# Optimization experiments

Measured on AMD Instinct MI355X. Metric: run time of the kernel, lower is better.

Reference implementation:

```python
import jax, jax.numpy as jnp
import numpy as np

B, T, L = 256, 1024, 128  # batch, seq_len, num_labels


def setup_inputs() -> dict:
    key = jax.random.key(0)
    k1, k2, k3, k4, k5 = jax.random.split(key, 5)
    h = jax.random.normal(k1, (B, T, L), dtype=jnp.float32)
    labels = jax.random.randint(k2, (B, T), 0, L)
    mask = jnp.ones((B, T), dtype=jnp.float32)
    u = lambda k, s: jax.random.uniform(k, s, jnp.float32, -0.1, 0.1)
    trans_matrix = u(k3, (L, L))
    start_trans = u(k4, (L,))
    end_trans = u(k5, (L,))
    return {"h": h, "labels": labels, "mask": mask,
            "trans_matrix": trans_matrix, "start_trans": start_trans,
            "end_trans": end_trans}


def reference(h, labels, mask, trans_matrix, start_trans, end_trans):
    # ---- numerator: score of the gold path ----
    h_y = jnp.take_along_axis(h, labels[..., None], axis=2)[..., 0]      # (B,T)
    trans_y = trans_matrix[labels[:, :-1], labels[:, 1:]]                # (B,T-1)
    num = start_trans[labels[:, 0]]
    num = num + jnp.sum(h_y[:, :-1] * mask[:, :-1] + trans_y * mask[:, 1:], axis=1)
    last_idx = mask.astype(jnp.int32).sum(axis=1) - 1                    # (B,)
    last_labels = jnp.take_along_axis(labels, last_idx[:, None], axis=1)[:, 0]
    # original torch code gathers from h[:, -1] (last timestep), keep faithful
    num = num + jnp.take_along_axis(h[:, -1], last_labels[:, None], axis=1)[:, 0] * mask[:, -1]
    num = num + end_trans[last_labels]

    # ---- denominator: log partition via scan over time ----
    def step(score, inp):
        h_t, m_t = inp  # (B,L), (B,)
        s = jax.nn.logsumexp(score[:, :, None] + h_t[:, None, :] + trans_matrix[None], axis=1)
        m = m_t[:, None]
        return s * m + score * (1.0 - m), None

    score0 = start_trans[None, :] + h[:, 0]                              # (B,L)
    hs = jnp.swapaxes(h, 0, 1)[1:]                                       # (T-1,B,L)
    ms = mask.T[1:]                                                      # (T-1,B)
    scoreT, _ = jax.lax.scan(step, score0, (hs, ms))
    den = jax.nn.logsumexp(scoreT + end_trans[None, :], axis=1)          # (B,)

    return num - den
```

## Files before the change

### kernel.cpp

```cpp
#include <hip/hip_runtime.h>
#include <math.h>

#define Bb 256
#define Tt 1024
#define Ll 128

typedef float v2f __attribute__((ext_vector_type(2)));

__global__ __launch_bounds__(256) void crf_expT_kernel(
    const float* __restrict__ trans, float* __restrict__ expT)
{
    int idx = blockIdx.x * 256 + threadIdx.x;
    if (idx < Ll * Ll) {
        int jj = idx >> 7;
        int ii = idx & (Ll - 1);
        expT[idx] = __expf(trans[ii * Ll + jj]);
    }
}

__global__ __launch_bounds__(256) void crf_num_kernel(
    const float* __restrict__ h, const int* __restrict__ labels,
    const float* __restrict__ mask, const float* __restrict__ trans,
    const float* __restrict__ start_trans, const float* __restrict__ end_trans,
    float* __restrict__ num_out)
{
    const int b = blockIdx.x;
    const int tid = threadIdx.x;
    const int* lab = labels + b * Tt;
    const float* mk = mask + b * Tt;
    const float* hb = h + (size_t)b * Tt * Ll;

    float acc = 0.f;
    float msum = 0.f;
    for (int t = tid; t < Tt; t += 256) {
        int lt = lab[t];
        float mt = mk[t];
        msum += mt;
        if (t < Tt - 1) {
            int lt1 = lab[t + 1];
            acc += hb[t * Ll + lt] * mt + trans[lt * Ll + lt1] * mk[t + 1];
        }
    }
    for (int off = 32; off; off >>= 1) {
        acc  += __shfl_down(acc, off, 64);
        msum += __shfl_down(msum, off, 64);
    }
    __shared__ float racc[4], rmsum[4];
    const int wave = tid >> 6;
    if ((tid & 63) == 0) { racc[wave] = acc; rmsum[wave] = msum; }
    __syncthreads();
    if (tid == 0) {
        float a = racc[0] + racc[1] + racc[2] + racc[3];
        float m = rmsum[0] + rmsum[1] + rmsum[2] + rmsum[3];
        int last_idx = (int)(m + 0.5f) - 1;
        if (last_idx < 0) last_idx = 0;
        if (last_idx > Tt - 1) last_idx = Tt - 1;
        int last_lab = lab[last_idx];
        float num = a + start_trans[lab[0]];
        num += hb[(Tt - 1) * Ll + last_lab] * mk[Tt - 1];
        num += end_trans[last_lab];
        num_out[b] = num;
    }
}

__global__ __launch_bounds__(256)
__attribute__((amdgpu_waves_per_eu(1, 1)))
void crf_den_kernel(
    const float* __restrict__ h, const float* __restrict__ mask,
    const float* __restrict__ expT, const float* __restrict__ start_trans,
    const float* __restrict__ end_trans, const float* __restrict__ num_in,
    float* __restrict__ out)
{
    __shared__ float p_lds[2][160];
    __shared__ float mk_lds[Tt];
    __shared__ float redm[4], reds[4];

    const int b = blockIdx.x;
    const int tid = threadIdx.x;
    const int wave = tid >> 6;
    const int lane = tid & 63;
    const int jgrp = lane >> 3;
    const int isl  = lane & 7;
    const int jbase = (wave << 5) + (jgrp << 2);
    const int wcol  = jbase + (isl & 3);
    const bool writer = (isl < 4);
    const int waddr = wcol + ((wcol >> 4) << 2);
    const bool lb0 = (lane & 1) != 0;
    const bool lb1 = (lane & 2) != 0;

    const float* hb = h + (size_t)b * Tt * Ll;
    const float* mk = mask + b * Tt;

    ((float4*)mk_lds)[tid] = ((const float4*)mk)[tid];

    const v2f* EAp = (const v2f*)(expT + (jbase + 0) * Ll + (isl << 4));
    const v2f* EBp = (const v2f*)(expT + (jbase + 1) * Ll + (isl << 4));
    const v2f* ECp = (const v2f*)(expT + (jbase + 2) * Ll + (isl << 4));
    const v2f* EDp = (const v2f*)(expT + (jbase + 3) * Ll + (isl << 4));
    v2f EA0=EAp[0],EA1=EAp[1],EA2=EAp[2],EA3=EAp[3],EA4=EAp[4],EA5=EAp[5],EA6=EAp[6],EA7=EAp[7];
    v2f EB0=EBp[0],EB1=EBp[1],EB2=EBp[2],EB3=EBp[3],EB4=EBp[4],EB5=EBp[5],EB6=EBp[6],EB7=EBp[7];
    v2f EC0=ECp[0],EC1=ECp[1],EC2=ECp[2],EC3=ECp[3],EC4=ECp[4],EC5=ECp[5],EC6=ECp[6],EC7=ECp[7];
    v2f ED0=EDp[0],ED1=EDp[1],ED2=EDp[2],ED3=EDp[3],ED4=EDp[4],ED5=EDp[5],ED6=EDp[6],ED7=EDp[7];

    float S = start_trans[0] + hb[0] + 16.0f;
    float score0 = start_trans[wcol] + hb[wcol];
    float pw = __expf(score0 - S);
    if (writer) p_lds[0][waddr] = pw;

    float h1 = hb[1 * Ll + wcol], m1 = mk[1];
    float h2 = hb[2 * Ll + wcol], m2 = mk[2];
    float h3 = hb[3 * Ll + wcol], m3 = mk[3];
    float h0 = hb[4 * Ll + wcol], m0 = mk[4];
    __syncthreads();

    float ex1 = __expf(h1) * m1, om1 = 1.f - m1;
    float ex0, om0, ex2, om2, ex3, om3;

#define DPPA(x, ctrl) __int_as_float(__builtin_amdgcn_update_dpp( \
        0, __float_as_int(x), ctrl, 0xF, 0xF, true))

#define BODY(RBUF, UPD, EXc, OMc, HN, MN, EXn, OMn, HR, MR, TR) {      \
    const float4* pp = (const float4*)(&p_lds[RBUF][isl * 20]);        \
    float4 Q0 = pp[0], Q1 = pp[1], Q2 = pp[2], Q3 = pp[3];             \
    float pz = 0.f;                                                    \
    if (UPD) pz = p_lds[RBUF][0];                                      \
    HR = hb[(TR) * Ll + wcol];                                         \
    MR = mk_lds[(TR)];                                                 \
    v2f q00 = {Q0.x,Q0.y}, q01 = {Q0.z,Q0.w};                          \
    v2f q10 = {Q1.x,Q1.y}, q11 = {Q1.z,Q1.w};                          \
    v2f q20 = {Q2.x,Q2.y}, q21 = {Q2.z,Q2.w};                          \
    v2f q30 = {Q3.x,Q3.y}, q31 = {Q3.z,Q3.w};                          \
    v2f A0 = q00*EA0; A0 = q01*EA1 + A0; A0 = q10*EA2 + A0;            \
    A0 = q11*EA3 + A0; A0 = q20*EA4 + A0; A0 = q21*EA5 + A0;           \
    A0 = q30*EA6 + A0; A0 = q31*EA7 + A0;                              \
    v2f A1 = q00*EB0; A1 = q01*EB1 + A1; A1 = q10*EB2 + A1;            \
    A1 = q11*EB3 + A1; A1 = q20*EB4 + A1; A1 = q21*EB5 + A1;           \
    A1 = q30*EB6 + A1; A1 = q31*EB7 + A1;                              \
    v2f A2 = q00*EC0; A2 = q01*EC1 + A2; A2 = q10*EC2 + A2;            \
    A2 = q11*EC3 + A2; A2 = q20*EC4 + A2; A2 = q21*EC5 + A2;           \
    A2 = q30*EC6 + A2; A2 = q31*EC7 + A2;                              \
    v2f A3 = q00*ED0; A3 = q01*ED1 + A3; A3 = q10*ED2 + A3;            \
    A3 = q11*ED3 + A3; A3 = q20*ED4 + A3; A3 = q21*ED5 + A3;           \
    A3 = q30*ED6 + A3; A3 = q31*ED7 + A3;                              \
    float a0 = A0.x + A0.y, a1 = A1.x + A1.y;                          \
    float a2 = A2.x + A2.y, a3 = A3.x + A3.y;                          \
    a0 += DPPA(a0, 0x141); a1 += DPPA(a1, 0x141);                      \
    a2 += DPPA(a2, 0x141); a3 += DPPA(a3, 0x141);                      \
    float u01 = lb0 ? a1 : a0, v01 = lb0 ? a0 : a1;                    \
    float b01 = u01 + DPPA(v01, 0xB1);                                 \
    float u23 = lb0 ? a3 : a2, v23 = lb0 ? a2 : a3;                    \
    float b23 = u23 + DPPA(v23, 0xB1);                                 \
    float uf = lb1 ? b23 : b01, vf = lb1 ? b01 : b23;                  \
    float acc = uf + DPPA(vf, 0x4E);                                   \
    float c1 = EXc, c0 = pw * OMc;                                     \
    if (UPD) { float ed = __fdividef(1.12535175e-7f, pz);              \
               c1 *= ed; c0 *= ed; S += __logf(pz) + 16.0f; }          \
    float pn = fmaf(acc, c1, c0);                                      \
    if (writer) p_lds[(RBUF) ^ 1][waddr] = pn;                         \
    EXn = __expf(HN) * MN; OMn = 1.f - MN;                             \
    pw = pn;                                                           \
    __builtin_amdgcn_sched_barrier(0);                                 \
    asm volatile("s_waitcnt lgkmcnt(0)");                              \
    __builtin_amdgcn_s_barrier();                                      \
    __builtin_amdgcn_sched_barrier(0);                                 \
}

    BODY(0, 0, ex1, om1, h2, m2, ex2, om2, h1, m1, 5)
    BODY(1, 0, ex2, om2, h3, m3, ex3, om3, h2, m2, 6)
    BODY(0, 0, ex3, om3, h0, m0, ex0, om0, h3, m3, 7)

    for (int k = 1; k < 255; ++k) {
        int t4 = k << 2;
        BODY(1, 1, ex0, om0, h1, m1, ex1, om1, h0, m0, t4 + 4)
        BODY(0, 0, ex1, om1, h2, m2, ex2, om2, h1, m1, t4 + 5)
        BODY(1, 0, ex2, om2, h3, m3, ex3, om3, h2, m2, t4 + 6)
        BODY(0, 0, ex3, om3, h0, m0, ex0, om0, h3, m3, t4 + 7)
    }
    BODY(1, 1, ex0, om0, h1, m1, ex1, om1, h0, m0, Tt - 1)
    BODY(0, 0, ex1, om1, h2, m2, ex2, om2, h1, m1, Tt - 1)
    BODY(1, 0, ex2, om2, h3, m3, ex3, om3, h2, m2, Tt - 1)
    BODY(0, 0, ex3, om3, h0, m0, ex0, om0, h3, m3, Tt - 1)
#undef BODY
#undef DPPA

    float v = __logf(pw) + S + end_trans[wcol];
    float mval = writer ? v : -1e30f;
    #pragma unroll
    for (int off = 32; off; off >>= 1) mval = fmaxf(mval, __shfl_xor(mval, off, 64));
    if (lane == 0) redm[wave] = mval;
    __syncthreads();
    float M = fmaxf(fmaxf(redm[0], redm[1]), fmaxf(redm[2], redm[3]));
    float e = writer ? __expf(v - M) : 0.f;
    #pragma unroll
    for (int off = 32; off; off >>= 1) e += __shfl_xor(e, off, 64);
    if (lane == 0) reds[wave] = e;
    __syncthreads();
    if (tid == 0) {
        float den = M + __logf(reds[0] + reds[1] + reds[2] + reds[3]);
        out[b] = num_in[b] - den;
    }
}

extern "C" void kernel_launch(void* const* d_in, const int* in_sizes, int n_in,
                              void* d_out, int out_size, void* d_ws, size_t ws_size,
                              hipStream_t stream) {
    const float* h           = (const float*)d_in[0];
    const int*   labels      = (const int*)d_in[1];
    const float* mask        = (const float*)d_in[2];
    const float* trans       = (const float*)d_in[3];
    const float* start_trans = (const float*)d_in[4];
    const float* end_trans   = (const float*)d_in[5];
    float* out    = (float*)d_out;
    float* num_ws = (float*)d_ws;
    float* expT   = (float*)d_ws + 256;

    crf_expT_kernel<<<(Ll * Ll + 255) / 256, 256, 0, stream>>>(trans, expT);
    crf_num_kernel<<<Bb, 256, 0, stream>>>(h, labels, mask, trans, start_trans, end_trans, num_ws);
    crf_den_kernel<<<Bb, 256, 0, stream>>>(h, mask, expT, start_trans, end_trans, num_ws, out);
}
```

Measured before the change: 264.4 us.

## Fuse exp-transition, numerator and forward-scan kernels into one launch

Merges the three kernels into one. Each block now computes exp(trans) straight from the transition matrix into its register tiles, computes the gold-path numerator before the scan, and reduces it with the denominator at the end. This removes two kernel launches and the workspace round trip for expT and num, at the cost of redundant exp work per block and strided global reads of trans. The scan also loads mask values four at a time as a float4 from LDS instead of one scalar LDS read per step.

After: 247.8 us. 1.07x faster.

```diff
diff --git a/kernel.cpp b/kernel.cpp
--- a/kernel.cpp
+++ b/kernel.cpp
@@ -7,73 +7,19 @@
 
 typedef float v2f __attribute__((ext_vector_type(2)));
 
-__global__ __launch_bounds__(256) void crf_expT_kernel(
-    const float* __restrict__ trans, float* __restrict__ expT)
-{
-    int idx = blockIdx.x * 256 + threadIdx.x;
-    if (idx < Ll * Ll) {
-        int jj = idx >> 7;
-        int ii = idx & (Ll - 1);
-        expT[idx] = __expf(trans[ii * Ll + jj]);
-    }
-}
+__device__ __forceinline__ v2f ev2(float a, float b) { v2f r; r.x = a; r.y = b; return r; }
 
-__global__ __launch_bounds__(256) void crf_num_kernel(
+__global__ __launch_bounds__(256)
+__attribute__((amdgpu_waves_per_eu(1, 1)))
+void crf_fused_kernel(
     const float* __restrict__ h, const int* __restrict__ labels,
     const float* __restrict__ mask, const float* __restrict__ trans,
     const float* __restrict__ start_trans, const float* __restrict__ end_trans,
-    float* __restrict__ num_out)
-{
-    const int b = blockIdx.x;
-    const int tid = threadIdx.x;
-    const int* lab = labels + b * Tt;
-    const float* mk = mask + b * Tt;
-    const float* hb = h + (size_t)b * Tt * Ll;
-
-    float acc = 0.f;
-    float msum = 0.f;
-    for (int t = tid; t < Tt; t += 256) {
-        int lt = lab[t];
-        float mt = mk[t];
-        msum += mt;
-        if (t < Tt - 1) {
-            int lt1 = lab[t + 1];
-            acc += hb[t * Ll + lt] * mt + trans[lt * Ll + lt1] * mk[t + 1];
-        }
-    }
-    for (int off = 32; off; off >>= 1) {
-        acc  += __shfl_down(acc, off, 64);
-        msum += __shfl_down(msum, off, 64);
-    }
-    __shared__ float racc[4], rmsum[4];
-    const int wave = tid >> 6;
-    if ((tid & 63) == 0) { racc[wave] = acc; rmsum[wave] = msum; }
-    __syncthreads();
-    if (tid == 0) {
-        float a = racc[0] + racc[1] + racc[2] + racc[3];
-        float m = rmsum[0] + rmsum[1] + rmsum[2] + rmsum[3];
-        int last_idx = (int)(m + 0.5f) - 1;
-        if (last_idx < 0) last_idx = 0;
-        if (last_idx > Tt - 1) last_idx = Tt - 1;
-        int last_lab = lab[last_idx];
-        float num = a + start_trans[lab[0]];
-        num += hb[(Tt - 1) * Ll + last_lab] * mk[Tt - 1];
-        num += end_trans[last_lab];
-        num_out[b] = num;
-    }
-}
-
-__global__ __launch_bounds__(256)
-__attribute__((amdgpu_waves_per_eu(1, 1)))
-void crf_den_kernel(
-    const float* __restrict__ h, const float* __restrict__ mask,
-    const float* __restrict__ expT, const float* __restrict__ start_trans,
-    const float* __restrict__ end_trans, const float* __restrict__ num_in,
     float* __restrict__ out)
 {
     __shared__ float p_lds[2][160];
-    __shared__ float mk_lds[Tt];
-    __shared__ float redm[4], reds[4];
+    __shared__ float mk_lds[Tt + 4];
+    __shared__ float redm[4], reds[4], racc[4], rmsum[4];
 
     const int b = blockIdx.x;
     const int tid = threadIdx.x;
@@ -90,17 +36,33 @@
 
     const float* hb = h + (size_t)b * Tt * Ll;
     const float* mk = mask + b * Tt;
+    const int* lab = labels + b * Tt;
 
     ((float4*)mk_lds)[tid] = ((const float4*)mk)[tid];
 
-    const v2f* EAp = (const v2f*)(expT + (jbase + 0) * Ll + (isl << 4));
-    const v2f* EBp = (const v2f*)(expT + (jbase + 1) * Ll + (isl << 4));
-    const v2f* ECp = (const v2f*)(expT + (jbase + 2) * Ll + (isl << 4));
-    const v2f* EDp = (const v2f*)(expT + (jbase + 3) * Ll + (isl << 4));
-    v2f EA0=EAp[0],EA1=EAp[1],EA2=EAp[2],EA3=EAp[3],EA4=EAp[4],EA5=EAp[5],EA6=EAp[6],EA7=EAp[7];
-    v2f EB0=EBp[0],EB1=EBp[1],EB2=EBp[2],EB3=EBp[3],EB4=EBp[4],EB5=EBp[5],EB6=EBp[6],EB7=EBp[7];
-    v2f EC0=ECp[0],EC1=ECp[1],EC2=ECp[2],EC3=ECp[3],EC4=ECp[4],EC5=ECp[5],EC6=ECp[6],EC7=ECp[7];
-    v2f ED0=EDp[0],ED1=EDp[1],ED2=EDp[2],ED3=EDp[3],ED4=EDp[4],ED5=EDp[5],ED6=EDp[6],ED7=EDp[7];
+    float nacc = 0.f, nms = 0.f;
+    #pragma unroll
+    for (int r = 0; r < 4; ++r) {
+        int t = tid + (r << 8);
+        float mt = mk[t];
+        nms += mt;
+        if (t < Tt - 1) {
+            int lt = lab[t], lt1 = lab[t + 1];
+            nacc += hb[t * Ll + lt] * mt + trans[lt * Ll + lt1] * mk[t + 1];
+        }
+    }
+
+    const float* tp = trans + (size_t)(isl << 4) * Ll + jbase;
+#define EXT2(k, c) ev2(__expf(tp[(2 * (k)) * Ll + (c)]), __expf(tp[(2 * (k) + 1) * Ll + (c)]))
+    v2f EA0=EXT2(0,0),EA1=EXT2(1,0),EA2=EXT2(2,0),EA3=EXT2(3,0),
+        EA4=EXT2(4,0),EA5=EXT2(5,0),EA6=EXT2(6,0),EA7=EXT2(7,0);
+    v2f EB0=EXT2(0,1),EB1=EXT2(1,1),EB2=EXT2(2,1),EB3=EXT2(3,1),
+        EB4=EXT2(4,1),EB5=EXT2(5,1),EB6=EXT2(6,1),EB7=EXT2(7,1);
+    v2f EC0=EXT2(0,2),EC1=EXT2(1,2),EC2=EXT2(2,2),EC3=EXT2(3,2),
+        EC4=EXT2(4,2),EC5=EXT2(5,2),EC6=EXT2(6,2),EC7=EXT2(7,2);
+    v2f ED0=EXT2(0,3),ED1=EXT2(1,3),ED2=EXT2(2,3),ED3=EXT2(3,3),
+        ED4=EXT2(4,3),ED5=EXT2(5,3),ED6=EXT2(6,3),ED7=EXT2(7,3);
+#undef EXT2
 
     float S = start_trans[0] + hb[0] + 16.0f;
     float score0 = start_trans[wcol] + hb[wcol];
@@ -115,17 +77,19 @@
 
     float ex1 = __expf(h1) * m1, om1 = 1.f - m1;
     float ex0, om0, ex2, om2, ex3, om3;
+    float4 MQ;
 
 #define DPPA(x, ctrl) __int_as_float(__builtin_amdgcn_update_dpp( \
         0, __float_as_int(x), ctrl, 0xF, 0xF, true))
 
-#define BODY(RBUF, UPD, EXc, OMc, HN, MN, EXn, OMn, HR, MR, TR) {      \
+#define BODY(RBUF, UPD, EXc, OMc, HN, MN, EXn, OMn, HR, MR, TR, MV, LQ) {  \
     const float4* pp = (const float4*)(&p_lds[RBUF][isl * 20]);        \
     float4 Q0 = pp[0], Q1 = pp[1], Q2 = pp[2], Q3 = pp[3];             \
     float pz = 0.f;                                                    \
     if (UPD) pz = p_lds[RBUF][0];                                      \
     HR = hb[(TR) * Ll + wcol];                                         \
-    MR = mk_lds[(TR)];                                                 \
+    MR = (MV);                                                         \
+    if (LQ) MQ = *(const float4*)(&mk_lds[(TR) + 1]);                  \
     v2f q00 = {Q0.x,Q0.y}, q01 = {Q0.z,Q0.w};                          \
     v2f q10 = {Q1.x,Q1.y}, q11 = {Q1.z,Q1.w};                          \
     v2f q20 = {Q2.x,Q2.y}, q21 = {Q2.z,Q2.w};                          \
@@ -165,29 +129,33 @@
     __builtin_amdgcn_sched_barrier(0);                                 \
 }
 
-    BODY(0, 0, ex1, om1, h2, m2, ex2, om2, h1, m1, 5)
-    BODY(1, 0, ex2, om2, h3, m3, ex3, om3, h2, m2, 6)
-    BODY(0, 0, ex3, om3, h0, m0, ex0, om0, h3, m3, 7)
+    BODY(0, 0, ex1, om1, h2, m2, ex2, om2, h1, m1, 5, mk_lds[5], 0)
+    BODY(1, 0, ex2, om2, h3, m3, ex3, om3, h2, m2, 6, mk_lds[6], 0)
+    BODY(0, 0, ex3, om3, h0, m0, ex0, om0, h3, m3, 7, mk_lds[7], 1)
 
     for (int k = 1; k < 255; ++k) {
         int t4 = k << 2;
-        BODY(1, 1, ex0, om0, h1, m1, ex1, om1, h0, m0, t4 + 4)
-        BODY(0, 0, ex1, om1, h2, m2, ex2, om2, h1, m1, t4 + 5)
-        BODY(1, 0, ex2, om2, h3, m3, ex3, om3, h2, m2, t4 + 6)
-        BODY(0, 0, ex3, om3, h0, m0, ex0, om0, h3, m3, t4 + 7)
+        BODY(1, 1, ex0, om0, h1, m1, ex1, om1, h0, m0, t4 + 4, MQ.x, 0)
+        BODY(0, 0, ex1, om1, h2, m2, ex2, om2, h1, m1, t4 + 5, MQ.y, 0)
+        BODY(1, 0, ex2, om2, h3, m3, ex3, om3, h2, m2, t4 + 6, MQ.z, 0)
+        BODY(0, 0, ex3, om3, h0, m0, ex0, om0, h3, m3, t4 + 7, MQ.w, 1)
     }
-    BODY(1, 1, ex0, om0, h1, m1, ex1, om1, h0, m0, Tt - 1)
-    BODY(0, 0, ex1, om1, h2, m2, ex2, om2, h1, m1, Tt - 1)
-    BODY(1, 0, ex2, om2, h3, m3, ex3, om3, h2, m2, Tt - 1)
-    BODY(0, 0, ex3, om3, h0, m0, ex0, om0, h3, m3, Tt - 1)
+    BODY(1, 1, ex0, om0, h1, m1, ex1, om1, h0, m0, Tt - 4, MQ.x, 0)
+    BODY(0, 0, ex1, om1, h2, m2, ex2, om2, h1, m1, Tt - 1, MQ.y, 0)
+    BODY(1, 0, ex2, om2, h3, m3, ex3, om3, h2, m2, Tt - 1, MQ.z, 0)
+    BODY(0, 0, ex3, om3, h0, m0, ex0, om0, h3, m3, Tt - 1, MQ.w, 0)
 #undef BODY
 #undef DPPA
 
     float v = __logf(pw) + S + end_trans[wcol];
     float mval = writer ? v : -1e30f;
     #pragma unroll
-    for (int off = 32; off; off >>= 1) mval = fmaxf(mval, __shfl_xor(mval, off, 64));
-    if (lane == 0) redm[wave] = mval;
+    for (int off = 32; off; off >>= 1) {
+        mval = fmaxf(mval, __shfl_xor(mval, off, 64));
+        nacc += __shfl_down(nacc, off, 64);
+        nms  += __shfl_down(nms,  off, 64);
+    }
+    if (lane == 0) { redm[wave] = mval; racc[wave] = nacc; rmsum[wave] = nms; }
     __syncthreads();
     float M = fmaxf(fmaxf(redm[0], redm[1]), fmaxf(redm[2], redm[3]));
     float e = writer ? __expf(v - M) : 0.f;
@@ -197,7 +165,16 @@
     __syncthreads();
     if (tid == 0) {
         float den = M + __logf(reds[0] + reds[1] + reds[2] + reds[3]);
-        out[b] = num_in[b] - den;
+        float a  = racc[0] + racc[1] + racc[2] + racc[3];
+        float mm = rmsum[0] + rmsum[1] + rmsum[2] + rmsum[3];
+        int last_idx = (int)(mm + 0.5f) - 1;
+        if (last_idx < 0) last_idx = 0;
+        if (last_idx > Tt - 1) last_idx = Tt - 1;
+        int last_lab = lab[last_idx];
+        float num = a + start_trans[lab[0]];
+        num += hb[(Tt - 1) * Ll + last_lab] * mk_lds[Tt - 1];
+        num += end_trans[last_lab];
+        out[b] = num - den;
     }
 }
 
@@ -210,11 +187,8 @@
     const float* trans       = (const float*)d_in[3];
     const float* start_trans = (const float*)d_in[4];
     const float* end_trans   = (const float*)d_in[5];
-    float* out    = (float*)d_out;
-    float* num_ws = (float*)d_ws;
-    float* expT   = (float*)d_ws + 256;
+    float* out = (float*)d_out;
 
-    crf_expT_kernel<<<(Ll * Ll + 255) / 256, 256, 0, stream>>>(trans, expT);
-    crf_num_kernel<<<Bb, 256, 0, stream>>>(h, labels, mask, trans, start_trans, end_trans, num_ws);
-    crf_den_kernel<<<Bb, 256, 0, stream>>>(h, mask, expT, start_trans, end_trans, num_ws, out);
+    crf_fused_kernel<<<Bb, 256, 0, stream>>>(h, labels, mask, trans,
+                                             start_trans, end_trans, out);
 }
```
